# Kernel tuning notes

Hardware: AMD Instinct MI355X
Metric: run time of the kernel (lower is better)

The kernel has to match this reference:

```python
import jax, jax.numpy as jnp
import numpy as np
import math

N, L, C, H, K = 4, 16384, 256, 8, 4
D = C // H


def setup_inputs():
    rng = jax.random.key(0)
    ks = jax.random.split(rng, 16)
    def w(k, shape, scale):
        return jax.random.normal(k, shape, jnp.float32) * scale
    s = 1.0 / math.sqrt(C)
    return {
        "query": jax.random.normal(ks[0], (N, L, C), jnp.float32),
        "key": jax.random.normal(ks[1], (N, L, C), jnp.float32),
        "value": jax.random.normal(ks[2], (N, L, C), jnp.float32),
        "reference_points": jax.random.uniform(ks[3], (N, L, 2), jnp.float32),
        "pos_embed": jax.random.normal(ks[4], (N, L, C), jnp.float32),
        "Wq": w(ks[5], (C, C), s), "bq": jnp.zeros((C,), jnp.float32),
        "Wk": w(ks[6], (C, C), s), "bk": jnp.zeros((C,), jnp.float32),
        "Wv": w(ks[7], (C, C), s), "bv": jnp.zeros((C,), jnp.float32),
        "Wo1": w(ks[8], (C, 2 * C), s), "bo1": jnp.zeros((2 * C,), jnp.float32),
        "Wo2": w(ks[9], (2 * C, H * K * 2), 0.02), "bo2": w(ks[10], (H * K * 2,), 0.02),
        "Wpos": w(ks[11], (C, C), s), "bpos": jnp.zeros((C,), jnp.float32),
        "Wout": w(ks[12], (C, C), s), "bout": jnp.zeros((C,), jnp.float32),
    }


def _sample_weight(points):
    # F.grid_sample on a 1x1 feature map (bilinear, zeros padding, align_corners=False)
    # degenerates to a scalar weight: grid g = 2p-1, unnormalized c = g/2 = p - 0.5,
    # pixel-0 bilinear weight per axis = max(0, 1 - |c|).
    c = points - 0.5
    return jax.nn.relu(1.0 - jnp.abs(c[..., 0])) * jax.nn.relu(1.0 - jnp.abs(c[..., 1]))


def reference(query, key, value, reference_points, pos_embed,
              Wq, bq, Wk, bk, Wv, bv, Wo1, bo1, Wo2, bo2, Wpos, bpos, Wout, bout):
    Nb, Ln, Cd = query.shape
    q = (query @ Wq + bq).reshape(Nb, Ln, H, D)
    k = (key @ Wk + bk).reshape(Nb, Ln, H, D)
    v = (value @ Wv + bv).reshape(Nb, Ln, H, D)
    pos = (pos_embed @ Wpos + bpos).reshape(Nb, Ln, H, D)
    q = q + pos
    k = k + pos
    # offset MLP: Linear(C,2C) -> ReLU -> Linear(2C, H*K*2)
    offsets = (jax.nn.relu(query @ Wo1 + bo1) @ Wo2 + bo2).reshape(Nb, Ln, H, K, 2)
    sp = reference_points[:, :, None, None, :] + offsets  # [N,L,H,K,2]
    w = _sample_weight(sp)                                # [N,L,H,K]
    # sampled_k[n,l,h,k,:] = k[n,l,h,:] * w[n,l,h,k]  (1x1 grid_sample closed form)
    qk = jnp.einsum('nlhd,nlhd->nlh', q, k)               # [N,L,H]
    attn = jax.nn.softmax(qk[..., None] * w / math.sqrt(D), axis=-1)  # [N,L,H,K]
    # output = sum_k attn_k * (v * w_k) = v * sum_k(attn_k * w_k)
    wv = jnp.sum(attn * w, axis=-1)                       # [N,L,H]
    out = (v * wv[..., None]).reshape(Nb, Ln, Cd)
    return out @ Wout + bout
```

## Files before the change

kernel.cpp:

```cpp
#include <hip/hip_runtime.h>
#include <hip/hip_bf16.h>

typedef __bf16 bf16x8 __attribute__((ext_vector_type(8)));
typedef float f32x4 __attribute__((ext_vector_type(4)));
typedef float f32x2 __attribute__((ext_vector_type(2)));

#define MT 64
#define CC 256

__device__ __forceinline__ int swz(int r, int c) {
    return r * 512 + ((c * 2) ^ ((r & 7) << 4));
}

__device__ __forceinline__ bf16x8 ldB(const __bf16* __restrict__ WT, int nc, int KC, int kc,
                                      int laneoff) {
    return *(const bf16x8*)(WT + ((size_t)nc * KC + kc) * 512 + laneoff);
}

__device__ __forceinline__ void stream_tile(const float* __restrict__ src, int row0, int tid,
                                            __bf16* dst) {
#pragma unroll
    for (int i = 0; i < 8; ++i) {
        int f = i * 512 + tid;
        int r = f >> 6;
        int c = (f & 63) * 4;
        f32x4 v = __builtin_nontemporal_load((const f32x4*)(src + (size_t)(row0 + r) * CC + c));
        union { __bf16 h[4]; unsigned long long u; } uu;
        uu.h[0] = (__bf16)v[0]; uu.h[1] = (__bf16)v[1];
        uu.h[2] = (__bf16)v[2]; uu.h[3] = (__bf16)v[3];
        *(unsigned long long*)((char*)dst + swz(r, c)) = uu.u;
    }
}

__global__ void prep_all(const float* __restrict__ Wq, const float* __restrict__ Wk,
                         const float* __restrict__ Wpos, const float* __restrict__ Wo1,
                         const float* __restrict__ Wo2, const float* __restrict__ Wv,
                         const float* __restrict__ Wout, __bf16* __restrict__ ws)
{
    int i = blockIdx.x * 256 + threadIdx.x;
    if (i >= 557056) return;
    int j, K, N;
    const float* S0 = nullptr; const float* S1 = nullptr;
    if (i < 131072)      { j = i;          K = 512; N = 256; S0 = Wq;  S1 = Wpos; }
    else if (i < 262144) { j = i - 131072; K = 512; N = 256; S0 = Wk;  S1 = Wpos; }
    else if (i < 393216) { j = i - 262144; K = 256; N = 512; S0 = Wo1; }
    else if (i < 425984) { j = i - 393216; K = 512; N = 64;  S0 = Wo2; }
    else if (i < 491520) { j = i - 425984; K = 256; N = 256; S0 = Wv; }
    else                 { j = i - 491520; K = 256; N = 256; S0 = Wout; }
    int tile = j >> 9, r = j & 511;
    int lane = r >> 3, e = r & 7;
    int q4 = lane >> 4, r16 = lane & 15;
    int KC = K >> 5;
    int nc = tile / KC, kc = tile - nc * KC;
    int k = kc * 32 + q4 * 8 + e;
    int n = nc * 16 + r16;
    float v;
    if (S1 && k >= 256) v = S1[(size_t)(k - 256) * N + n];
    else                v = S0[(size_t)k * N + n];
    ws[i] = (__bf16)v;
}

extern "C" __global__ void __launch_bounds__(512, 2)
fused_ext_attn(const float* __restrict__ query, const float* __restrict__ key,
               const float* __restrict__ value, const float* __restrict__ refp,
               const float* __restrict__ pose,
               const __bf16* __restrict__ ws,
               const float* __restrict__ bq, const float* __restrict__ bk,
               const float* __restrict__ bv, const float* __restrict__ bpos,
               const float* __restrict__ bo1, const float* __restrict__ bo2,
               const float* __restrict__ bout,
               float* __restrict__ out)
{
    const __bf16* WTqp  = ws;
    const __bf16* WTkp  = ws + 131072;
    const __bf16* WTo1  = ws + 262144;
    const __bf16* WTo2  = ws + 393216;
    const __bf16* WTv   = ws + 425984;
    const __bf16* WTout = ws + 491520;

    __shared__ __attribute__((aligned(16))) __bf16 SA[MT * CC];
    __shared__ __attribute__((aligned(16))) __bf16 SX[MT * CC];
    __shared__ __attribute__((aligned(16))) char   SY[12288];

    __bf16* off_b = (__bf16*)SY;
    float*  qk_s  = (float*)(SY + 8192);
    float*  wv_s  = (float*)(SY + 10240);

    const int tid = threadIdx.x;
    const int lane = tid & 63;
    const int wid = tid >> 6;
    const int r16 = lane & 15;
    const int q4 = lane >> 4;
    const int laneoff = lane * 8;
    const int row0 = blockIdx.x * MT;

    stream_tile(query, row0, tid, SA);
    __syncthreads();

    f32x4 accO[4];
#pragma unroll
    for (int i = 0; i < 4; ++i) accO[i] = (f32x4){0.f, 0.f, 0.f, 0.f};
    for (int p = 0; p < 2; ++p) {
        f32x4 acc[4][2];
#pragma unroll
        for (int i = 0; i < 4; ++i)
#pragma unroll
            for (int j = 0; j < 2; ++j) acc[i][j] = (f32x4){0.f, 0.f, 0.f, 0.f};
#pragma unroll
        for (int ks = 0; ks < 8; ++ks) {
            int ak = ks * 32 + q4 * 8;
            bf16x8 a[4], b[2];
#pragma unroll
            for (int mf = 0; mf < 4; ++mf)
                a[mf] = *(const bf16x8*)((const char*)SA + swz(mf * 16 + r16, ak));
#pragma unroll
            for (int nf = 0; nf < 2; ++nf)
                b[nf] = ldB(WTo1, p * 16 + wid * 2 + nf, 8, ks, laneoff);
#pragma unroll
            for (int mf = 0; mf < 4; ++mf)
#pragma unroll
                for (int nf = 0; nf < 2; ++nf)
                    acc[mf][nf] = __builtin_amdgcn_mfma_f32_16x16x32_bf16(a[mf], b[nf], acc[mf][nf], 0, 0, 0);
        }
#pragma unroll
        for (int mf = 0; mf < 4; ++mf)
#pragma unroll
            for (int nf = 0; nf < 2; ++nf) {
                int col = wid * 32 + nf * 16 + r16;
                float bias = bo1[p * 256 + col];
#pragma unroll
                for (int r = 0; r < 4; ++r)
                    *(__bf16*)((char*)SX + swz(mf * 16 + q4 * 4 + r, col)) =
                        (__bf16)fmaxf(acc[mf][nf][r] + bias, 0.f);
            }
        __syncthreads();
        if (wid < 4) {
#pragma unroll
            for (int ks = 0; ks < 8; ++ks) {
                int ak = ks * 32 + q4 * 8;
                bf16x8 b = ldB(WTo2, wid, 16, p * 8 + ks, laneoff);
#pragma unroll
                for (int mf = 0; mf < 4; ++mf) {
                    bf16x8 a = *(const bf16x8*)((const char*)SX + swz(mf * 16 + r16, ak));
                    accO[mf] = __builtin_amdgcn_mfma_f32_16x16x32_bf16(a, b, accO[mf], 0, 0, 0);
                }
            }
            if (p == 1) {
                int col = wid * 16 + r16;
                float b2 = bo2[col];
#pragma unroll
                for (int mf = 0; mf < 4; ++mf)
#pragma unroll
                    for (int r = 0; r < 4; ++r)
                        off_b[(mf * 16 + q4 * 4 + r) * 64 + col] = (__bf16)(accO[mf][r] + b2);
            }
        }
        __syncthreads();
    }

    f32x4 qa[4][2];
#pragma unroll
    for (int i = 0; i < 4; ++i)
#pragma unroll
        for (int j = 0; j < 2; ++j) qa[i][j] = (f32x4){0.f, 0.f, 0.f, 0.f};
    stream_tile(pose, row0, tid, SX);
#pragma unroll
    for (int ks = 0; ks < 8; ++ks) {
        int ak = ks * 32 + q4 * 8;
        bf16x8 a[4], b[2];
#pragma unroll
        for (int mf = 0; mf < 4; ++mf)
            a[mf] = *(const bf16x8*)((const char*)SA + swz(mf * 16 + r16, ak));
#pragma unroll
        for (int nf = 0; nf < 2; ++nf)
            b[nf] = ldB(WTqp, wid * 2 + nf, 16, ks, laneoff);
#pragma unroll
        for (int mf = 0; mf < 4; ++mf)
#pragma unroll
            for (int nf = 0; nf < 2; ++nf)
                qa[mf][nf] = __builtin_amdgcn_mfma_f32_16x16x32_bf16(a[mf], b[nf], qa[mf][nf], 0, 0, 0);
    }
    __syncthreads();

    stream_tile(key, row0, tid, SA);
#pragma unroll
    for (int ks = 8; ks < 16; ++ks) {
        int ak = (ks - 8) * 32 + q4 * 8;
        bf16x8 a[4], b[2];
#pragma unroll
        for (int mf = 0; mf < 4; ++mf)
            a[mf] = *(const bf16x8*)((const char*)SX + swz(mf * 16 + r16, ak));
#pragma unroll
        for (int nf = 0; nf < 2; ++nf)
            b[nf] = ldB(WTqp, wid * 2 + nf, 16, ks, laneoff);
#pragma unroll
        for (int mf = 0; mf < 4; ++mf)
#pragma unroll
            for (int nf = 0; nf < 2; ++nf)
                qa[mf][nf] = __builtin_amdgcn_mfma_f32_16x16x32_bf16(a[mf], b[nf], qa[mf][nf], 0, 0, 0);
    }
    __syncthreads();

    {
        f32x4 ka[4][2];
#pragma unroll
        for (int i = 0; i < 4; ++i)
#pragma unroll
            for (int j = 0; j < 2; ++j) ka[i][j] = (f32x4){0.f, 0.f, 0.f, 0.f};
#pragma unroll
        for (int ks = 0; ks < 16; ++ks) {
            int ak = (ks & 7) * 32 + q4 * 8;
            const char* Abase = (ks < 8) ? (const char*)SA : (const char*)SX;
            bf16x8 a[4], b[2];
#pragma unroll
            for (int mf = 0; mf < 4; ++mf)
                a[mf] = *(const bf16x8*)(Abase + swz(mf * 16 + r16, ak));
#pragma unroll
            for (int nf = 0; nf < 2; ++nf)
                b[nf] = ldB(WTkp, wid * 2 + nf, 16, ks, laneoff);
#pragma unroll
            for (int mf = 0; mf < 4; ++mf)
#pragma unroll
                for (int nf = 0; nf < 2; ++nf)
                    ka[mf][nf] = __builtin_amdgcn_mfma_f32_16x16x32_bf16(a[mf], b[nf], ka[mf][nf], 0, 0, 0);
        }
        float Bq[2], Bk[2];
#pragma unroll
        for (int nf = 0; nf < 2; ++nf) {
            int col = wid * 32 + nf * 16 + r16;
            Bq[nf] = bq[col] + bpos[col];
            Bk[nf] = bk[col] + bpos[col];
        }
#pragma unroll
        for (int mf = 0; mf < 4; ++mf)
#pragma unroll
            for (int r = 0; r < 4; ++r) {
                float p0 = (qa[mf][0][r] + Bq[0]) * (ka[mf][0][r] + Bk[0])
                         + (qa[mf][1][r] + Bq[1]) * (ka[mf][1][r] + Bk[1]);
#pragma unroll
                for (int m = 1; m < 16; m <<= 1)
                    p0 += __shfl_xor(p0, m);
                if (r16 == 0)
                    qk_s[(mf * 16 + q4 * 4 + r) * 8 + wid] = p0;
            }
    }
    __syncthreads();

    stream_tile(value, row0, tid, SA);
    {
        int t = tid >> 3, h = tid & 7;
        float qk = qk_s[t * 8 + h];
        f32x2 rp = __builtin_nontemporal_load((const f32x2*)(refp + (size_t)(row0 + t) * 2));
        float wgt[4], lg[4];
        float m = -1e30f;
#pragma unroll
        for (int kk = 0; kk < 4; ++kk) {
            float ox = (float)off_b[t * 64 + (h * 4 + kk) * 2];
            float oy = (float)off_b[t * 64 + (h * 4 + kk) * 2 + 1];
            float cx = rp[0] + ox - 0.5f, cy = rp[1] + oy - 0.5f;
            float wx = fmaxf(0.f, 1.f - fabsf(cx));
            float wy = fmaxf(0.f, 1.f - fabsf(cy));
            wgt[kk] = wx * wy;
            lg[kk] = qk * wgt[kk] * 0.17677669529663687f;
            m = fmaxf(m, lg[kk]);
        }
        float s = 0.f, sw = 0.f;
#pragma unroll
        for (int kk = 0; kk < 4; ++kk) {
            float e = __expf(lg[kk] - m);
            s += e;
            sw += e * wgt[kk];
        }
        wv_s[t * 8 + h] = sw / s;
    }
    __syncthreads();

    {
        f32x4 acc[4][2];
#pragma unroll
        for (int i = 0; i < 4; ++i)
#pragma unroll
            for (int j = 0; j < 2; ++j) acc[i][j] = (f32x4){0.f, 0.f, 0.f, 0.f};
#pragma unroll
        for (int ks = 0; ks < 8; ++ks) {
            int ak = ks * 32 + q4 * 8;
            bf16x8 a[4], b[2];
#pragma unroll
            for (int mf = 0; mf < 4; ++mf)
                a[mf] = *(const bf16x8*)((const char*)SA + swz(mf * 16 + r16, ak));
#pragma unroll
            for (int nf = 0; nf < 2; ++nf)
                b[nf] = ldB(WTv, wid * 2 + nf, 8, ks, laneoff);
#pragma unroll
            for (int mf = 0; mf < 4; ++mf)
#pragma unroll
                for (int nf = 0; nf < 2; ++nf)
                    acc[mf][nf] = __builtin_amdgcn_mfma_f32_16x16x32_bf16(a[mf], b[nf], acc[mf][nf], 0, 0, 0);
        }
#pragma unroll
        for (int mf = 0; mf < 4; ++mf)
#pragma unroll
            for (int nf = 0; nf < 2; ++nf) {
                int col = wid * 32 + nf * 16 + r16;
                float bias = bv[col];
#pragma unroll
                for (int r = 0; r < 4; ++r) {
                    int row = mf * 16 + q4 * 4 + r;
                    float wvv = wv_s[row * 8 + wid];
                    *(__bf16*)((char*)SX + swz(row, col)) = (__bf16)((acc[mf][nf][r] + bias) * wvv);
                }
            }
    }
    __syncthreads();

    {
        f32x4 acc[4][2];
#pragma unroll
        for (int i = 0; i < 4; ++i)
#pragma unroll
            for (int j = 0; j < 2; ++j) acc[i][j] = (f32x4){0.f, 0.f, 0.f, 0.f};
#pragma unroll
        for (int ks = 0; ks < 8; ++ks) {
            int ak = ks * 32 + q4 * 8;
            bf16x8 a[4], b[2];
#pragma unroll
            for (int mf = 0; mf < 4; ++mf)
                a[mf] = *(const bf16x8*)((const char*)SX + swz(mf * 16 + r16, ak));
#pragma unroll
            for (int nf = 0; nf < 2; ++nf)
                b[nf] = ldB(WTout, wid * 2 + nf, 8, ks, laneoff);
#pragma unroll
            for (int mf = 0; mf < 4; ++mf)
#pragma unroll
                for (int nf = 0; nf < 2; ++nf)
                    acc[mf][nf] = __builtin_amdgcn_mfma_f32_16x16x32_bf16(a[mf], b[nf], acc[mf][nf], 0, 0, 0);
        }
#pragma unroll
        for (int mf = 0; mf < 4; ++mf)
#pragma unroll
            for (int nf = 0; nf < 2; ++nf) {
                int col = wid * 32 + nf * 16 + r16;
                float bias = bout[col];
#pragma unroll
                for (int r = 0; r < 4; ++r) {
                    int row = mf * 16 + q4 * 4 + r;
                    __builtin_nontemporal_store(acc[mf][nf][r] + bias,
                                                out + (size_t)(row0 + row) * CC + col);
                }
            }
    }
}

extern "C" void kernel_launch(void* const* d_in, const int* in_sizes, int n_in,
                              void* d_out, int out_size, void* d_ws, size_t ws_size,
                              hipStream_t stream)
{
    const float* query = (const float*)d_in[0];
    const float* key   = (const float*)d_in[1];
    const float* value = (const float*)d_in[2];
    const float* refp  = (const float*)d_in[3];
    const float* pose  = (const float*)d_in[4];
    const float* Wq  = (const float*)d_in[5];  const float* bq   = (const float*)d_in[6];
    const float* Wk  = (const float*)d_in[7];  const float* bk   = (const float*)d_in[8];
    const float* Wv  = (const float*)d_in[9];  const float* bv   = (const float*)d_in[10];
    const float* Wo1 = (const float*)d_in[11]; const float* bo1  = (const float*)d_in[12];
    const float* Wo2 = (const float*)d_in[13]; const float* bo2  = (const float*)d_in[14];
    const float* Wpos= (const float*)d_in[15]; const float* bpos = (const float*)d_in[16];
    const float* Wout= (const float*)d_in[17]; const float* bout = (const float*)d_in[18];

    __bf16* ws = (__bf16*)d_ws;

    prep_all<<<2176, 256, 0, stream>>>(Wq, Wk, Wpos, Wo1, Wo2, Wv, Wout, ws);

    fused_ext_attn<<<65536 / MT, 512, 0, stream>>>(
        query, key, value, refp, pose, ws,
        bq, bk, bv, bpos, bo1, bo2, bout, (float*)d_out);
}
```

Before: 138.4 us.

## Shrink LDS footprint and prefetch next input tiles into registers

Replaces the second 32KB LDS tile with a 16KB half-width hidden buffer by splitting the offset MLP into four 128-column passes spread across all eight waves. Pose, key and value tiles are loaded into registers ahead of time and written to the single shared tile later, so global loads overlap with MFMA work. The concatenated [q;pos] and [k;pos] weights become separate Wq, Wk and Wpos matrices, and pos@Wpos is computed once and added to both accumulators. The lower LDS use may allow more blocks per CU, at the cost of extra barriers, more register pressure from the staged tiles, and one extra MFMA pass over pos.

```diff
diff --git a/kernel.cpp b/kernel.cpp
--- a/kernel.cpp
+++ b/kernel.cpp
@@ -11,25 +11,44 @@
 __device__ __forceinline__ int swz(int r, int c) {
     return r * 512 + ((c * 2) ^ ((r & 7) << 4));
 }
+__device__ __forceinline__ int swzH(int r, int c) {
+    return r * 256 + ((c * 2) ^ ((r & 7) << 4));
+}
 
 __device__ __forceinline__ bf16x8 ldB(const __bf16* __restrict__ WT, int nc, int KC, int kc,
                                       int laneoff) {
     return *(const bf16x8*)(WT + ((size_t)nc * KC + kc) * 512 + laneoff);
 }
 
-__device__ __forceinline__ void stream_tile(const float* __restrict__ src, int row0, int tid,
-                                            __bf16* dst) {
+__device__ __forceinline__ void stage_issue(const float* __restrict__ src, int row0, int tid,
+                                            unsigned long long (&h)[8]) {
 #pragma unroll
     for (int i = 0; i < 8; ++i) {
         int f = i * 512 + tid;
         int r = f >> 6;
         int c = (f & 63) * 4;
         f32x4 v = __builtin_nontemporal_load((const f32x4*)(src + (size_t)(row0 + r) * CC + c));
-        union { __bf16 h[4]; unsigned long long u; } uu;
-        uu.h[0] = (__bf16)v[0]; uu.h[1] = (__bf16)v[1];
-        uu.h[2] = (__bf16)v[2]; uu.h[3] = (__bf16)v[3];
-        *(unsigned long long*)((char*)dst + swz(r, c)) = uu.u;
-    }
+        union { __bf16 b[4]; unsigned long long u; } uu;
+        uu.b[0] = (__bf16)v[0]; uu.b[1] = (__bf16)v[1];
+        uu.b[2] = (__bf16)v[2]; uu.b[3] = (__bf16)v[3];
+        h[i] = uu.u;
+    }
+}
+__device__ __forceinline__ void stage_retire(__bf16* dst, int tid,
+                                             const unsigned long long (&h)[8]) {
+#pragma unroll
+    for (int i = 0; i < 8; ++i) {
+        int f = i * 512 + tid;
+        int r = f >> 6;
+        int c = (f & 63) * 4;
+        *(unsigned long long*)((char*)dst + swz(r, c)) = h[i];
+    }
+}
+__device__ __forceinline__ void stream_tile(const float* __restrict__ src, int row0, int tid,
+                                            __bf16* dst) {
+    unsigned long long h[8];
+    stage_issue(src, row0, tid, h);
+    stage_retire(dst, tid, h);
 }
 
 __global__ void prep_all(const float* __restrict__ Wq, const float* __restrict__ Wk,
@@ -38,15 +57,16 @@
                          const float* __restrict__ Wout, __bf16* __restrict__ ws)
 {
     int i = blockIdx.x * 256 + threadIdx.x;
-    if (i >= 557056) return;
+    if (i >= 491520) return;
     int j, K, N;
-    const float* S0 = nullptr; const float* S1 = nullptr;
-    if (i < 131072)      { j = i;          K = 512; N = 256; S0 = Wq;  S1 = Wpos; }
-    else if (i < 262144) { j = i - 131072; K = 512; N = 256; S0 = Wk;  S1 = Wpos; }
-    else if (i < 393216) { j = i - 262144; K = 256; N = 512; S0 = Wo1; }
-    else if (i < 425984) { j = i - 393216; K = 512; N = 64;  S0 = Wo2; }
-    else if (i < 491520) { j = i - 425984; K = 256; N = 256; S0 = Wv; }
-    else                 { j = i - 491520; K = 256; N = 256; S0 = Wout; }
+    const float* S0;
+    if (i < 65536)       { j = i;          K = 256; N = 256; S0 = Wq; }
+    else if (i < 131072) { j = i - 65536;  K = 256; N = 256; S0 = Wk; }
+    else if (i < 196608) { j = i - 131072; K = 256; N = 256; S0 = Wpos; }
+    else if (i < 327680) { j = i - 196608; K = 256; N = 512; S0 = Wo1; }
+    else if (i < 360448) { j = i - 327680; K = 512; N = 64;  S0 = Wo2; }
+    else if (i < 425984) { j = i - 360448; K = 256; N = 256; S0 = Wv; }
+    else                 { j = i - 425984; K = 256; N = 256; S0 = Wout; }
     int tile = j >> 9, r = j & 511;
     int lane = r >> 3, e = r & 7;
     int q4 = lane >> 4, r16 = lane & 15;
@@ -54,10 +74,7 @@
     int nc = tile / KC, kc = tile - nc * KC;
     int k = kc * 32 + q4 * 8 + e;
     int n = nc * 16 + r16;
-    float v;
-    if (S1 && k >= 256) v = S1[(size_t)(k - 256) * N + n];
-    else                v = S0[(size_t)k * N + n];
-    ws[i] = (__bf16)v;
+    ws[i] = (__bf16)S0[(size_t)k * N + n];
 }
 
 extern "C" __global__ void __launch_bounds__(512, 2)
@@ -71,15 +88,16 @@
                const float* __restrict__ bout,
                float* __restrict__ out)
 {
-    const __bf16* WTqp  = ws;
-    const __bf16* WTkp  = ws + 131072;
-    const __bf16* WTo1  = ws + 262144;
-    const __bf16* WTo2  = ws + 393216;
-    const __bf16* WTv   = ws + 425984;
-    const __bf16* WTout = ws + 491520;
+    const __bf16* WTq   = ws;
+    const __bf16* WTk   = ws + 65536;
+    const __bf16* WTpos = ws + 131072;
+    const __bf16* WTo1  = ws + 196608;
+    const __bf16* WTo2  = ws + 327680;
+    const __bf16* WTv   = ws + 360448;
+    const __bf16* WTout = ws + 425984;
 
     __shared__ __attribute__((aligned(16))) __bf16 SA[MT * CC];
-    __shared__ __attribute__((aligned(16))) __bf16 SX[MT * CC];
+    __shared__ __attribute__((aligned(16))) __bf16 H[MT * 128];
     __shared__ __attribute__((aligned(16))) char   SY[12288];
 
     __bf16* off_b = (__bf16*)SY;
@@ -94,76 +112,70 @@
     const int laneoff = lane * 8;
     const int row0 = blockIdx.x * MT;
 
+    unsigned long long hpose[8];
     stream_tile(query, row0, tid, SA);
-    __syncthreads();
-
-    f32x4 accO[4];
-#pragma unroll
-    for (int i = 0; i < 4; ++i) accO[i] = (f32x4){0.f, 0.f, 0.f, 0.f};
-    for (int p = 0; p < 2; ++p) {
-        f32x4 acc[4][2];
-#pragma unroll
-        for (int i = 0; i < 4; ++i)
-#pragma unroll
-            for (int j = 0; j < 2; ++j) acc[i][j] = (f32x4){0.f, 0.f, 0.f, 0.f};
+    stage_issue(pose, row0, tid, hpose);
+    __syncthreads();
+
+    f32x4 accO[2];
+    accO[0] = (f32x4){0.f, 0.f, 0.f, 0.f};
+    accO[1] = (f32x4){0.f, 0.f, 0.f, 0.f};
+    const int oc = wid & 3;
+    const int rbase = (wid >> 2) * 32;
+    for (int p = 0; p < 4; ++p) {
+        f32x4 acc[4];
+#pragma unroll
+        for (int i = 0; i < 4; ++i) acc[i] = (f32x4){0.f, 0.f, 0.f, 0.f};
 #pragma unroll
         for (int ks = 0; ks < 8; ++ks) {
             int ak = ks * 32 + q4 * 8;
-            bf16x8 a[4], b[2];
+            bf16x8 b = ldB(WTo1, p * 8 + wid, 8, ks, laneoff);
+#pragma unroll
+            for (int mf = 0; mf < 4; ++mf) {
+                bf16x8 a = *(const bf16x8*)((const char*)SA + swz(mf * 16 + r16, ak));
+                acc[mf] = __builtin_amdgcn_mfma_f32_16x16x32_bf16(a, b, acc[mf], 0, 0, 0);
+            }
+        }
+        {
+            int lcol = wid * 16 + r16;
+            float bias = bo1[p * 128 + lcol];
 #pragma unroll
             for (int mf = 0; mf < 4; ++mf)
-                a[mf] = *(const bf16x8*)((const char*)SA + swz(mf * 16 + r16, ak));
-#pragma unroll
-            for (int nf = 0; nf < 2; ++nf)
-                b[nf] = ldB(WTo1, p * 16 + wid * 2 + nf, 8, ks, laneoff);
-#pragma unroll
-            for (int mf = 0; mf < 4; ++mf)
-#pragma unroll
-                for (int nf = 0; nf < 2; ++nf)
-                    acc[mf][nf] = __builtin_amdgcn_mfma_f32_16x16x32_bf16(a[mf], b[nf], acc[mf][nf], 0, 0, 0);
-        }
-#pragma unroll
-        for (int mf = 0; mf < 4; ++mf)
-#pragma unroll
-            for (int nf = 0; nf < 2; ++nf) {
-                int col = wid * 32 + nf * 16 + r16;
-                float bias = bo1[p * 256 + col];
 #pragma unroll
                 for (int r = 0; r < 4; ++r)
-                    *(__bf16*)((char*)SX + swz(mf * 16 + q4 * 4 + r, col)) =
-                        (__bf16)fmaxf(acc[mf][nf][r] + bias, 0.f);
-            }
+                    *(__bf16*)((char*)H + swzH(mf * 16 + q4 * 4 + r, lcol)) =
+                        (__bf16)fmaxf(acc[mf][r] + bias, 0.f);
+        }
         __syncthreads();
-        if (wid < 4) {
-#pragma unroll
-            for (int ks = 0; ks < 8; ++ks) {
-                int ak = ks * 32 + q4 * 8;
-                bf16x8 b = ldB(WTo2, wid, 16, p * 8 + ks, laneoff);
-#pragma unroll
-                for (int mf = 0; mf < 4; ++mf) {
-                    bf16x8 a = *(const bf16x8*)((const char*)SX + swz(mf * 16 + r16, ak));
-                    accO[mf] = __builtin_amdgcn_mfma_f32_16x16x32_bf16(a, b, accO[mf], 0, 0, 0);
-                }
-            }
-            if (p == 1) {
-                int col = wid * 16 + r16;
-                float b2 = bo2[col];
-#pragma unroll
-                for (int mf = 0; mf < 4; ++mf)
-#pragma unroll
-                    for (int r = 0; r < 4; ++r)
-                        off_b[(mf * 16 + q4 * 4 + r) * 64 + col] = (__bf16)(accO[mf][r] + b2);
+#pragma unroll
+        for (int ks = 0; ks < 4; ++ks) {
+            int ak = ks * 32 + q4 * 8;
+            bf16x8 b = ldB(WTo2, oc, 16, p * 4 + ks, laneoff);
+#pragma unroll
+            for (int mf = 0; mf < 2; ++mf) {
+                bf16x8 a = *(const bf16x8*)((const char*)H + swzH(rbase + mf * 16 + r16, ak));
+                accO[mf] = __builtin_amdgcn_mfma_f32_16x16x32_bf16(a, b, accO[mf], 0, 0, 0);
             }
         }
         __syncthreads();
     }
-
+    {
+        int col = oc * 16 + r16;
+        float b2 = bo2[col];
+#pragma unroll
+        for (int mf = 0; mf < 2; ++mf)
+#pragma unroll
+            for (int r = 0; r < 4; ++r)
+                off_b[(rbase + mf * 16 + q4 * 4 + r) * 64 + col] = (__bf16)(accO[mf][r] + b2);
+    }
+
+    unsigned long long hkey[8];
+    stage_issue(key, row0, tid, hkey);
     f32x4 qa[4][2];
 #pragma unroll
     for (int i = 0; i < 4; ++i)
 #pragma unroll
         for (int j = 0; j < 2; ++j) qa[i][j] = (f32x4){0.f, 0.f, 0.f, 0.f};
-    stream_tile(pose, row0, tid, SX);
 #pragma unroll
     for (int ks = 0; ks < 8; ++ks) {
         int ak = ks * 32 + q4 * 8;
@@ -173,7 +185,7 @@
             a[mf] = *(const bf16x8*)((const char*)SA + swz(mf * 16 + r16, ak));
 #pragma unroll
         for (int nf = 0; nf < 2; ++nf)
-            b[nf] = ldB(WTqp, wid * 2 + nf, 16, ks, laneoff);
+            b[nf] = ldB(WTq, wid * 2 + nf, 8, ks, laneoff);
 #pragma unroll
         for (int mf = 0; mf < 4; ++mf)
 #pragma unroll
@@ -182,48 +194,58 @@
     }
     __syncthreads();
 
-    stream_tile(key, row0, tid, SA);
-#pragma unroll
-    for (int ks = 8; ks < 16; ++ks) {
-        int ak = (ks - 8) * 32 + q4 * 8;
+    stage_retire(SA, tid, hpose);
+    __syncthreads();
+
+    f32x4 pk[4][2];
+#pragma unroll
+    for (int i = 0; i < 4; ++i)
+#pragma unroll
+        for (int j = 0; j < 2; ++j) pk[i][j] = (f32x4){0.f, 0.f, 0.f, 0.f};
+#pragma unroll
+    for (int ks = 0; ks < 8; ++ks) {
+        int ak = ks * 32 + q4 * 8;
         bf16x8 a[4], b[2];
 #pragma unroll
         for (int mf = 0; mf < 4; ++mf)
-            a[mf] = *(const bf16x8*)((const char*)SX + swz(mf * 16 + r16, ak));
+            a[mf] = *(const bf16x8*)((const char*)SA + swz(mf * 16 + r16, ak));
 #pragma unroll
         for (int nf = 0; nf < 2; ++nf)
-            b[nf] = ldB(WTqp, wid * 2 + nf, 16, ks, laneoff);
-#pragma unroll
-        for (int mf = 0; mf < 4; ++mf)
-#pragma unroll
-            for (int nf = 0; nf < 2; ++nf)
-                qa[mf][nf] = __builtin_amdgcn_mfma_f32_16x16x32_bf16(a[mf], b[nf], qa[mf][nf], 0, 0, 0);
-    }
-    __syncthreads();
-
+            b[nf] = ldB(WTpos, wid * 2 + nf, 8, ks, laneoff);
+#pragma unroll
+        for (int mf = 0; mf < 4; ++mf)
+#pragma unroll
+            for (int nf = 0; nf < 2; ++nf)
+                pk[mf][nf] = __builtin_amdgcn_mfma_f32_16x16x32_bf16(a[mf], b[nf], pk[mf][nf], 0, 0, 0);
+    }
+#pragma unroll
+    for (int i = 0; i < 4; ++i)
+#pragma unroll
+        for (int j = 0; j < 2; ++j) qa[i][j] += pk[i][j];
+    __syncthreads();
+
+    stage_retire(SA, tid, hkey);
+    __syncthreads();
+
+    unsigned long long hval[8];
+    stage_issue(value, row0, tid, hval);
+#pragma unroll
+    for (int ks = 0; ks < 8; ++ks) {
+        int ak = ks * 32 + q4 * 8;
+        bf16x8 a[4], b[2];
+#pragma unroll
+        for (int mf = 0; mf < 4; ++mf)
+            a[mf] = *(const bf16x8*)((const char*)SA + swz(mf * 16 + r16, ak));
+#pragma unroll
+        for (int nf = 0; nf < 2; ++nf)
+            b[nf] = ldB(WTk, wid * 2 + nf, 8, ks, laneoff);
+#pragma unroll
+        for (int mf = 0; mf < 4; ++mf)
+#pragma unroll
+            for (int nf = 0; nf < 2; ++nf)
+                pk[mf][nf] = __builtin_amdgcn_mfma_f32_16x16x32_bf16(a[mf], b[nf], pk[mf][nf], 0, 0, 0);
+    }
     {
-        f32x4 ka[4][2];
-#pragma unroll
-        for (int i = 0; i < 4; ++i)
-#pragma unroll
-            for (int j = 0; j < 2; ++j) ka[i][j] = (f32x4){0.f, 0.f, 0.f, 0.f};
-#pragma unroll
-        for (int ks = 0; ks < 16; ++ks) {
-            int ak = (ks & 7) * 32 + q4 * 8;
-            const char* Abase = (ks < 8) ? (const char*)SA : (const char*)SX;
-            bf16x8 a[4], b[2];
-#pragma unroll
-            for (int mf = 0; mf < 4; ++mf)
-                a[mf] = *(const bf16x8*)(Abase + swz(mf * 16 + r16, ak));
-#pragma unroll
-            for (int nf = 0; nf < 2; ++nf)
-                b[nf] = ldB(WTkp, wid * 2 + nf, 16, ks, laneoff);
-#pragma unroll
-            for (int mf = 0; mf < 4; ++mf)
-#pragma unroll
-                for (int nf = 0; nf < 2; ++nf)
-                    ka[mf][nf] = __builtin_amdgcn_mfma_f32_16x16x32_bf16(a[mf], b[nf], ka[mf][nf], 0, 0, 0);
-        }
         float Bq[2], Bk[2];
 #pragma unroll
         for (int nf = 0; nf < 2; ++nf) {
@@ -235,8 +257,8 @@
         for (int mf = 0; mf < 4; ++mf)
 #pragma unroll
             for (int r = 0; r < 4; ++r) {
-                float p0 = (qa[mf][0][r] + Bq[0]) * (ka[mf][0][r] + Bk[0])
-                         + (qa[mf][1][r] + Bq[1]) * (ka[mf][1][r] + Bk[1]);
+                float p0 = (qa[mf][0][r] + Bq[0]) * (pk[mf][0][r] + Bk[0])
+                         + (qa[mf][1][r] + Bq[1]) * (pk[mf][1][r] + Bk[1]);
 #pragma unroll
                 for (int m = 1; m < 16; m <<= 1)
                     p0 += __shfl_xor(p0, m);
@@ -246,7 +268,7 @@
     }
     __syncthreads();
 
-    stream_tile(value, row0, tid, SA);
+    stage_retire(SA, tid, hval);
     {
         int t = tid >> 3, h = tid & 7;
         float qk = qk_s[t * 8 + h];
@@ -275,6 +297,43 @@
     }
     __syncthreads();
 
+    f32x4 vac[4][2];
+#pragma unroll
+    for (int i = 0; i < 4; ++i)
+#pragma unroll
+        for (int j = 0; j < 2; ++j) vac[i][j] = (f32x4){0.f, 0.f, 0.f, 0.f};
+#pragma unroll
+    for (int ks = 0; ks < 8; ++ks) {
+        int ak = ks * 32 + q4 * 8;
+        bf16x8 a[4], b[2];
+#pragma unroll
+        for (int mf = 0; mf < 4; ++mf)
+            a[mf] = *(const bf16x8*)((const char*)SA + swz(mf * 16 + r16, ak));
+#pragma unroll
+        for (int nf = 0; nf < 2; ++nf)
+            b[nf] = ldB(WTv, wid * 2 + nf, 8, ks, laneoff);
+#pragma unroll
+        for (int mf = 0; mf < 4; ++mf)
+#pragma unroll
+            for (int nf = 0; nf < 2; ++nf)
+                vac[mf][nf] = __builtin_amdgcn_mfma_f32_16x16x32_bf16(a[mf], b[nf], vac[mf][nf], 0, 0, 0);
+    }
+    __syncthreads();
+#pragma unroll
+    for (int mf = 0; mf < 4; ++mf)
+#pragma unroll
+        for (int nf = 0; nf < 2; ++nf) {
+            int col = wid * 32 + nf * 16 + r16;
+            float bias = bv[col];
+#pragma unroll
+            for (int r = 0; r < 4; ++r) {
+                int row = mf * 16 + q4 * 4 + r;
+                float wvv = wv_s[row * 8 + wid];
+                *(__bf16*)((char*)SA + swz(row, col)) = (__bf16)((vac[mf][nf][r] + bias) * wvv);
+            }
+        }
+    __syncthreads();
+
     {
         f32x4 acc[4][2];
 #pragma unroll
@@ -288,44 +347,6 @@
 #pragma unroll
             for (int mf = 0; mf < 4; ++mf)
                 a[mf] = *(const bf16x8*)((const char*)SA + swz(mf * 16 + r16, ak));
-#pragma unroll
-            for (int nf = 0; nf < 2; ++nf)
-                b[nf] = ldB(WTv, wid * 2 + nf, 8, ks, laneoff);
-#pragma unroll
-            for (int mf = 0; mf < 4; ++mf)
-#pragma unroll
-                for (int nf = 0; nf < 2; ++nf)
-                    acc[mf][nf] = __builtin_amdgcn_mfma_f32_16x16x32_bf16(a[mf], b[nf], acc[mf][nf], 0, 0, 0);
-        }
-#pragma unroll
-        for (int mf = 0; mf < 4; ++mf)
-#pragma unroll
-            for (int nf = 0; nf < 2; ++nf) {
-                int col = wid * 32 + nf * 16 + r16;
-                float bias = bv[col];
-#pragma unroll
-                for (int r = 0; r < 4; ++r) {
-                    int row = mf * 16 + q4 * 4 + r;
-                    float wvv = wv_s[row * 8 + wid];
-                    *(__bf16*)((char*)SX + swz(row, col)) = (__bf16)((acc[mf][nf][r] + bias) * wvv);
-                }
-            }
-    }
-    __syncthreads();
-
-    {
-        f32x4 acc[4][2];
-#pragma unroll
-        for (int i = 0; i < 4; ++i)
-#pragma unroll
-            for (int j = 0; j < 2; ++j) acc[i][j] = (f32x4){0.f, 0.f, 0.f, 0.f};
-#pragma unroll
-        for (int ks = 0; ks < 8; ++ks) {
-            int ak = ks * 32 + q4 * 8;
-            bf16x8 a[4], b[2];
-#pragma unroll
-            for (int mf = 0; mf < 4; ++mf)
-                a[mf] = *(const bf16x8*)((const char*)SX + swz(mf * 16 + r16, ak));
 #pragma unroll
             for (int nf = 0; nf < 2; ++nf)
                 b[nf] = ldB(WTout, wid * 2 + nf, 8, ks, laneoff);
@@ -370,7 +391,7 @@
 
     __bf16* ws = (__bf16*)d_ws;
 
-    prep_all<<<2176, 256, 0, stream>>>(Wq, Wk, Wpos, Wo1, Wo2, Wv, Wout, ws);
+    prep_all<<<1920, 256, 0, stream>>>(Wq, Wk, Wpos, Wo1, Wo2, Wv, Wout, ws);
 
     fused_ext_attn<<<65536 / MT, 512, 0, stream>>>(
         query, key, value, refp, pose, ws,
```

Result: slower. 142.1 us (+2.6%).

## Prefetch key/value tiles into registers during GEMMs and batch offset MLP

Applied to the files above, without the earlier changes.

Splits tile staging into a register-load phase and an LDS-store phase so the key and value global loads are issued before the preceding MFMA loops and retired afterwards, hiding memory latency behind compute. Adds a full 64x512 hidden buffer so the first offset-MLP layer is computed for both halves before the second layer runs once across all 8 waves (instead of 4 waves twice), removing two barriers. Loads query and pos tiles together up front. The extra LDS (~140KB) and register staging force launch bounds down to one block per CU, trading occupancy for overlap.

```diff
diff --git a/kernel.cpp b/kernel.cpp
--- a/kernel.cpp
+++ b/kernel.cpp
@@ -11,25 +11,44 @@
 __device__ __forceinline__ int swz(int r, int c) {
     return r * 512 + ((c * 2) ^ ((r & 7) << 4));
 }
+__device__ __forceinline__ int swzH(int r, int c) {
+    return r * 1024 + ((c * 2) ^ ((r & 7) << 4));
+}
 
 __device__ __forceinline__ bf16x8 ldB(const __bf16* __restrict__ WT, int nc, int KC, int kc,
                                       int laneoff) {
     return *(const bf16x8*)(WT + ((size_t)nc * KC + kc) * 512 + laneoff);
 }
 
-__device__ __forceinline__ void stream_tile(const float* __restrict__ src, int row0, int tid,
-                                            __bf16* dst) {
+__device__ __forceinline__ void stage_issue(const float* __restrict__ src, int row0, int tid,
+                                            unsigned long long (&h)[8]) {
 #pragma unroll
     for (int i = 0; i < 8; ++i) {
         int f = i * 512 + tid;
         int r = f >> 6;
         int c = (f & 63) * 4;
         f32x4 v = __builtin_nontemporal_load((const f32x4*)(src + (size_t)(row0 + r) * CC + c));
-        union { __bf16 h[4]; unsigned long long u; } uu;
-        uu.h[0] = (__bf16)v[0]; uu.h[1] = (__bf16)v[1];
-        uu.h[2] = (__bf16)v[2]; uu.h[3] = (__bf16)v[3];
-        *(unsigned long long*)((char*)dst + swz(r, c)) = uu.u;
-    }
+        union { __bf16 b[4]; unsigned long long u; } uu;
+        uu.b[0] = (__bf16)v[0]; uu.b[1] = (__bf16)v[1];
+        uu.b[2] = (__bf16)v[2]; uu.b[3] = (__bf16)v[3];
+        h[i] = uu.u;
+    }
+}
+__device__ __forceinline__ void stage_retire(__bf16* dst, int tid,
+                                             const unsigned long long (&h)[8]) {
+#pragma unroll
+    for (int i = 0; i < 8; ++i) {
+        int f = i * 512 + tid;
+        int r = f >> 6;
+        int c = (f & 63) * 4;
+        *(unsigned long long*)((char*)dst + swz(r, c)) = h[i];
+    }
+}
+__device__ __forceinline__ void stream_tile(const float* __restrict__ src, int row0, int tid,
+                                            __bf16* dst) {
+    unsigned long long h[8];
+    stage_issue(src, row0, tid, h);
+    stage_retire(dst, tid, h);
 }
 
 __global__ void prep_all(const float* __restrict__ Wq, const float* __restrict__ Wk,
@@ -60,7 +79,7 @@
     ws[i] = (__bf16)v;
 }
 
-extern "C" __global__ void __launch_bounds__(512, 2)
+extern "C" __global__ void __launch_bounds__(512, 1)
 fused_ext_attn(const float* __restrict__ query, const float* __restrict__ key,
                const float* __restrict__ value, const float* __restrict__ refp,
                const float* __restrict__ pose,
@@ -78,8 +97,9 @@
     const __bf16* WTv   = ws + 425984;
     const __bf16* WTout = ws + 491520;
 
-    __shared__ __attribute__((aligned(16))) __bf16 SA[MT * CC];
-    __shared__ __attribute__((aligned(16))) __bf16 SX[MT * CC];
+    __shared__ __attribute__((aligned(16))) __bf16 Q[MT * CC];
+    __shared__ __attribute__((aligned(16))) __bf16 P[MT * CC];
+    __shared__ __attribute__((aligned(16))) __bf16 H[MT * 512];
     __shared__ __attribute__((aligned(16))) char   SY[12288];
 
     __bf16* off_b = (__bf16*)SY;
@@ -94,12 +114,10 @@
     const int laneoff = lane * 8;
     const int row0 = blockIdx.x * MT;
 
-    stream_tile(query, row0, tid, SA);
-    __syncthreads();
-
-    f32x4 accO[4];
-#pragma unroll
-    for (int i = 0; i < 4; ++i) accO[i] = (f32x4){0.f, 0.f, 0.f, 0.f};
+    stream_tile(query, row0, tid, Q);
+    stream_tile(pose, row0, tid, P);
+    __syncthreads();
+
     for (int p = 0; p < 2; ++p) {
         f32x4 acc[4][2];
 #pragma unroll
@@ -112,7 +130,7 @@
             bf16x8 a[4], b[2];
 #pragma unroll
             for (int mf = 0; mf < 4; ++mf)
-                a[mf] = *(const bf16x8*)((const char*)SA + swz(mf * 16 + r16, ak));
+                a[mf] = *(const bf16x8*)((const char*)Q + swz(mf * 16 + r16, ak));
 #pragma unroll
             for (int nf = 0; nf < 2; ++nf)
                 b[nf] = ldB(WTo1, p * 16 + wid * 2 + nf, 8, ks, laneoff);
@@ -126,51 +144,31 @@
         for (int mf = 0; mf < 4; ++mf)
 #pragma unroll
             for (int nf = 0; nf < 2; ++nf) {
-                int col = wid * 32 + nf * 16 + r16;
-                float bias = bo1[p * 256 + col];
+                int col = p * 256 + wid * 32 + nf * 16 + r16;
+                float bias = bo1[col];
 #pragma unroll
                 for (int r = 0; r < 4; ++r)
-                    *(__bf16*)((char*)SX + swz(mf * 16 + q4 * 4 + r, col)) =
+                    *(__bf16*)((char*)H + swzH(mf * 16 + q4 * 4 + r, col)) =
                         (__bf16)fmaxf(acc[mf][nf][r] + bias, 0.f);
             }
-        __syncthreads();
-        if (wid < 4) {
-#pragma unroll
-            for (int ks = 0; ks < 8; ++ks) {
-                int ak = ks * 32 + q4 * 8;
-                bf16x8 b = ldB(WTo2, wid, 16, p * 8 + ks, laneoff);
-#pragma unroll
-                for (int mf = 0; mf < 4; ++mf) {
-                    bf16x8 a = *(const bf16x8*)((const char*)SX + swz(mf * 16 + r16, ak));
-                    accO[mf] = __builtin_amdgcn_mfma_f32_16x16x32_bf16(a, b, accO[mf], 0, 0, 0);
-                }
-            }
-            if (p == 1) {
-                int col = wid * 16 + r16;
-                float b2 = bo2[col];
-#pragma unroll
-                for (int mf = 0; mf < 4; ++mf)
-#pragma unroll
-                    for (int r = 0; r < 4; ++r)
-                        off_b[(mf * 16 + q4 * 4 + r) * 64 + col] = (__bf16)(accO[mf][r] + b2);
-            }
-        }
-        __syncthreads();
-    }
-
+    }
+    __syncthreads();
+
+    unsigned long long hkey[8];
+    stage_issue(key, row0, tid, hkey);
     f32x4 qa[4][2];
 #pragma unroll
     for (int i = 0; i < 4; ++i)
 #pragma unroll
         for (int j = 0; j < 2; ++j) qa[i][j] = (f32x4){0.f, 0.f, 0.f, 0.f};
-    stream_tile(pose, row0, tid, SX);
-#pragma unroll
-    for (int ks = 0; ks < 8; ++ks) {
-        int ak = ks * 32 + q4 * 8;
+#pragma unroll
+    for (int ks = 0; ks < 16; ++ks) {
+        int ak = (ks & 7) * 32 + q4 * 8;
+        const char* Abase = (ks < 8) ? (const char*)Q : (const char*)P;
         bf16x8 a[4], b[2];
 #pragma unroll
         for (int mf = 0; mf < 4; ++mf)
-            a[mf] = *(const bf16x8*)((const char*)SA + swz(mf * 16 + r16, ak));
+            a[mf] = *(const bf16x8*)(Abase + swz(mf * 16 + r16, ak));
 #pragma unroll
         for (int nf = 0; nf < 2; ++nf)
             b[nf] = ldB(WTqp, wid * 2 + nf, 16, ks, laneoff);
@@ -182,25 +180,35 @@
     }
     __syncthreads();
 
-    stream_tile(key, row0, tid, SA);
-#pragma unroll
-    for (int ks = 8; ks < 16; ++ks) {
-        int ak = (ks - 8) * 32 + q4 * 8;
-        bf16x8 a[4], b[2];
-#pragma unroll
-        for (int mf = 0; mf < 4; ++mf)
-            a[mf] = *(const bf16x8*)((const char*)SX + swz(mf * 16 + r16, ak));
-#pragma unroll
-        for (int nf = 0; nf < 2; ++nf)
-            b[nf] = ldB(WTqp, wid * 2 + nf, 16, ks, laneoff);
-#pragma unroll
-        for (int mf = 0; mf < 4; ++mf)
-#pragma unroll
-            for (int nf = 0; nf < 2; ++nf)
-                qa[mf][nf] = __builtin_amdgcn_mfma_f32_16x16x32_bf16(a[mf], b[nf], qa[mf][nf], 0, 0, 0);
-    }
-    __syncthreads();
-
+    stage_retire(Q, tid, hkey);
+    {
+        const int oc = wid & 3;
+        const int rbase = (wid >> 2) * 32;
+        f32x4 accO[2];
+        accO[0] = (f32x4){0.f, 0.f, 0.f, 0.f};
+        accO[1] = (f32x4){0.f, 0.f, 0.f, 0.f};
+#pragma unroll
+        for (int ks = 0; ks < 16; ++ks) {
+            int ak = ks * 32 + q4 * 8;
+            bf16x8 b = ldB(WTo2, oc, 16, ks, laneoff);
+#pragma unroll
+            for (int mf = 0; mf < 2; ++mf) {
+                bf16x8 a = *(const bf16x8*)((const char*)H + swzH(rbase + mf * 16 + r16, ak));
+                accO[mf] = __builtin_amdgcn_mfma_f32_16x16x32_bf16(a, b, accO[mf], 0, 0, 0);
+            }
+        }
+        int col = oc * 16 + r16;
+        float b2 = bo2[col];
+#pragma unroll
+        for (int mf = 0; mf < 2; ++mf)
+#pragma unroll
+            for (int r = 0; r < 4; ++r)
+                off_b[(rbase + mf * 16 + q4 * 4 + r) * 64 + col] = (__bf16)(accO[mf][r] + b2);
+    }
+    __syncthreads();
+
+    unsigned long long hval[8];
+    stage_issue(value, row0, tid, hval);
     {
         f32x4 ka[4][2];
 #pragma unroll
@@ -210,7 +218,7 @@
 #pragma unroll
         for (int ks = 0; ks < 16; ++ks) {
             int ak = (ks & 7) * 32 + q4 * 8;
-            const char* Abase = (ks < 8) ? (const char*)SA : (const char*)SX;
+            const char* Abase = (ks < 8) ? (const char*)Q : (const char*)P;
             bf16x8 a[4], b[2];
 #pragma unroll
             for (int mf = 0; mf < 4; ++mf)
@@ -246,7 +254,7 @@
     }
     __syncthreads();
 
-    stream_tile(value, row0, tid, SA);
+    stage_retire(Q, tid, hval);
     {
         int t = tid >> 3, h = tid & 7;
         float qk = qk_s[t * 8 + h];
@@ -287,7 +295,7 @@
             bf16x8 a[4], b[2];
 #pragma unroll
             for (int mf = 0; mf < 4; ++mf)
-                a[mf] = *(const bf16x8*)((const char*)SA + swz(mf * 16 + r16, ak));
+                a[mf] = *(const bf16x8*)((const char*)Q + swz(mf * 16 + r16, ak));
 #pragma unroll
             for (int nf = 0; nf < 2; ++nf)
                 b[nf] = ldB(WTv, wid * 2 + nf, 8, ks, laneoff);
@@ -307,7 +315,7 @@
                 for (int r = 0; r < 4; ++r) {
                     int row = mf * 16 + q4 * 4 + r;
                     float wvv = wv_s[row * 8 + wid];
-                    *(__bf16*)((char*)SX + swz(row, col)) = (__bf16)((acc[mf][nf][r] + bias) * wvv);
+                    *(__bf16*)((char*)P + swz(row, col)) = (__bf16)((acc[mf][nf][r] + bias) * wvv);
                 }
             }
     }
@@ -325,7 +333,7 @@
             bf16x8 a[4], b[2];
 #pragma unroll
             for (int mf = 0; mf < 4; ++mf)
-                a[mf] = *(const bf16x8*)((const char*)SX + swz(mf * 16 + r16, ak));
+                a[mf] = *(const bf16x8*)((const char*)P + swz(mf * 16 + r16, ak));
 #pragma unroll
             for (int nf = 0; nf < 2; ++nf)
                 b[nf] = ldB(WTout, wid * 2 + nf, 8, ks, laneoff);
```

After: 237.8 us. +71.8%, slower.
